# Kernel optimization log

Measured on AMD Instinct MI355X. Metric: run time of the kernel, lower is better.

The kernel has to match this reference:

```python
import jax, jax.numpy as jnp
import numpy as np

EPS = 1e-5
HEADS, K, U, M = 4, 16, 1, 11


def _bn(z, gamma, beta, mean, var):
    # z: [b, c, n]; BN in eval mode (running stats)
    inv = jax.lax.rsqrt(var + EPS)
    return (z - mean[None, :, None]) * (gamma * inv)[None, :, None] + beta[None, :, None]


def setup_inputs() -> dict:
    key = jax.random.key(0)
    ks = jax.random.split(key, 16)
    b, C, w, h = 8, 256, 64, 64
    vv = 256 // HEADS  # out_channels // heads = 64
    inp = {}
    inp['x'] = jax.random.normal(ks[0], (b, C, w, h), dtype=jnp.float32)
    sc = 1.0 / np.sqrt(C)
    inp['Wq'] = jax.random.normal(ks[1], (K * HEADS, C), dtype=jnp.float32) * sc
    inp['q_gamma'] = jnp.ones((K * HEADS,), jnp.float32)
    inp['q_beta'] = jnp.zeros((K * HEADS,), jnp.float32)
    inp['q_mean'] = jax.random.normal(ks[2], (K * HEADS,), dtype=jnp.float32) * 0.1
    inp['q_var'] = jax.random.uniform(ks[3], (K * HEADS,), minval=0.5, maxval=1.5, dtype=jnp.float32)
    inp['Wk'] = jax.random.normal(ks[4], (K * U, C), dtype=jnp.float32) * sc
    inp['Wv'] = jax.random.normal(ks[5], (vv * U, C), dtype=jnp.float32) * sc
    inp['v_gamma'] = jnp.ones((vv * U,), jnp.float32)
    inp['v_beta'] = jnp.zeros((vv * U,), jnp.float32)
    inp['v_mean'] = jax.random.normal(ks[6], (vv * U,), dtype=jnp.float32) * 0.1
    inp['v_var'] = jax.random.uniform(ks[7], (vv * U,), minval=0.5, maxval=1.5, dtype=jnp.float32)
    inp['embedding'] = jax.random.normal(ks[8], (K, U, 1, M, M), dtype=jnp.float32)
    return inp


def reference(x, Wq, q_gamma, q_beta, q_mean, q_var, Wk, Wv,
              v_gamma, v_beta, v_mean, v_var, embedding):
    b, C, w, h = x.shape
    n = w * h
    vv = Wv.shape[0] // U
    xf = x.reshape(b, C, n)

    # queries: 1x1 conv + BN -> [b, heads, k, n]
    q = _bn(jnp.einsum('oc,bcn->bon', Wq, xf), q_gamma, q_beta, q_mean, q_var)
    q = q.reshape(b, HEADS, K, n)

    # keys: 1x1 conv, softmax over spatial positions -> [b, k, u, n]
    keys = jnp.einsum('oc,bcn->bon', Wk, xf).reshape(b, K, U, n)
    sm = jax.nn.softmax(keys, axis=-1)

    # values: 1x1 conv + BN -> [b, vv, u, n]
    values = _bn(jnp.einsum('oc,bcn->bon', Wv, xf), v_gamma, v_beta, v_mean, v_var)
    values = values.reshape(b, vv, U, n)

    # content lambda
    lam_c = jnp.einsum('bkun,bvun->bkv', sm, values)          # [b, k, vv]
    y_c = jnp.einsum('bhkn,bkv->bhvn', q, lam_c)              # [b, h, vv, n]

    # position lambda via conv3d over (vv, w, h) with kernel (1, m, m)
    v5 = values.reshape(b, U, vv, w, h)                       # torch .view reinterpret
    pad = (M - 1) // 2
    lam_p = jax.lax.conv_general_dilated(
        v5, embedding, window_strides=(1, 1, 1),
        padding=((0, 0), (pad, pad), (pad, pad)),
        dimension_numbers=('NCDHW', 'OIDHW', 'NCDHW'))        # [b, k, vv, w, h]
    lam_p = lam_p.reshape(b, K, vv, n)
    y_p = jnp.einsum('bhkn,bkvn->bhvn', q, lam_p)             # [b, h, vv, n]

    out = (y_c + y_p).reshape(b, HEADS * vv, w, h)
    return out
```

## Files before the change

kernel.cpp:

```cpp
#include <hip/hip_runtime.h>
#include <math.h>

#define EPSBN 1e-5f

constexpr int B_ = 8, C_ = 256, N_ = 4096, IMG_ = 64;
constexpr int HEADS_ = 4, K_ = 16, VV_ = 64, M_ = 11, OC_ = 144;

typedef _Float16 half4 __attribute__((ext_vector_type(4)));
typedef _Float16 half8 __attribute__((ext_vector_type(8)));
typedef __fp16 fp16x2 __attribute__((ext_vector_type(2)));
typedef float f32x4 __attribute__((ext_vector_type(4)));

constexpr size_t O_WT   = 0;
constexpr size_t O_BIAS = 18432;
constexpr size_t O_EMBT = 18688;
constexpr size_t O_Q    = 24832;
constexpr size_t O_KEYS = O_Q    + 1048576;
constexpr size_t O_SM   = O_KEYS + 524288;
constexpr size_t O_VP   = O_SM   + 524288;
constexpr size_t O_VT16 = O_VP   + 1802240;
constexpr size_t O_LCP  = O_VT16 + 1048576;
constexpr size_t O_LC   = O_LCP  + 131072;

constexpr int VPROW = 88, VPPLANE = 80 * 88;

__global__ void k_prep(const float* __restrict__ Wq,
                       const float* __restrict__ qg, const float* __restrict__ qb,
                       const float* __restrict__ qm, const float* __restrict__ qv,
                       const float* __restrict__ Wk, const float* __restrict__ Wv,
                       const float* __restrict__ vg, const float* __restrict__ vb,
                       const float* __restrict__ vm, const float* __restrict__ vva,
                       const float* __restrict__ emb, float* __restrict__ ws) {
    int t = threadIdx.x, blk = blockIdx.x;
    _Float16* wf = (_Float16*)(ws + O_WT);
    int base = blk * 2304;
#pragma unroll
    for (int i = 0; i < 9; i++) {
        int idx = base + i * 256 + t;
        int o = idx >> 8, c = idx & 255;
        float w;
        if (o < 64) {
            float s = qg[o] * rsqrtf(qv[o] + EPSBN);
            w = Wq[o * 256 + c] * s;
        } else if (o < 80) {
            w = Wk[(o - 64) * 256 + c];
        } else {
            int ov = o - 80;
            float s = vg[ov] * rsqrtf(vva[ov] + EPSBN);
            w = Wv[ov * 256 + c] * s;
        }
        wf[idx] = (_Float16)w;
    }
    if (blk == 0 && t < 144) {
        float bias;
        if (t < 64) {
            float s = qg[t] * rsqrtf(qv[t] + EPSBN);
            bias = qb[t] - qm[t] * s;
        } else if (t < 80) {
            bias = 0.f;
        } else {
            int ov = t - 80;
            float s = vg[ov] * rsqrtf(vva[ov] + EPSBN);
            bias = vb[ov] - vm[ov] * s;
        }
        ws[O_BIAS + t] = bias;
    }
    if (blk == 15) {
        _Float16* ef = (_Float16*)(ws + O_EMBT);
        for (int idx = t; idx < 64 * 48; idx += 256) {
            int l = idx / 48, rem = idx % 48;
            int dp = rem >> 3, j = rem & 7;
            int k = l & 15, g = l >> 4;
            int dy = 2 * dp + (j >> 2);
            int dx = 4 * g + (j & 3);
            float v = (dy < 11 && dx < 11) ? emb[k * 121 + dy * 11 + dx] : 0.f;
            ef[idx] = (_Float16)v;
        }
    }
}

__global__ void k_zero(float* __restrict__ ws) {
    size_t i = (size_t)blockIdx.x * 256 + threadIdx.x;
    f32x4 z = {0.f, 0.f, 0.f, 0.f};
    *(f32x4*)(ws + O_VP + i * 4) = z;
}

__global__ __launch_bounds__(256) void k_proj(const float* __restrict__ x,
                                              const float* __restrict__ wsc,
                                              float* __restrict__ ws) {
    __shared__ uint WL[144 * 68];
    __shared__ uint XL[64 * 68];
    int b    = blockIdx.y;
    int pos0 = blockIdx.x * 64;
    int t    = threadIdx.x;
    int w = t >> 6, l = t & 63;
    int g = l >> 4, r = l & 15;

    f32x4 acc[9];
#pragma unroll
    for (int mf = 0; mf < 9; mf++) acc[mf] = (f32x4){0.f, 0.f, 0.f, 0.f};

    const uint* wsrc = (const uint*)(wsc + O_WT);
    const float* xb = x + (size_t)b * C_ * N_ + pos0;
    union u2h { uint2 u; half4 h; };

    for (int kh = 0; kh < 2; kh++) {
        if (kh) __syncthreads();
#pragma unroll
        for (int i = 0; i < 9; i++) {
            int idx = t + i * 256;
            int o = idx >> 4, c4 = idx & 15;
            uint4 wv = *(const uint4*)(wsrc + o * 128 + kh * 64 + c4 * 4);
            *(uint4*)&WL[o * 68 + c4 * 4] = wv;
        }
#pragma unroll
        for (int i = 0; i < 4; i++) {
            int idx = t + i * 256;
            int cl = idx >> 4, p4 = idx & 15;
            float4 a0 = *(const float4*)(xb + (size_t)(2 * (64 * kh + cl)) * N_ + 4 * p4);
            float4 a1 = *(const float4*)(xb + (size_t)(2 * (64 * kh + cl) + 1) * N_ + 4 * p4);
            union { _Float16 h[2]; uint u; } pk;
#pragma unroll
            for (int j = 0; j < 4; j++) {
                float v0 = (j == 0) ? a0.x : (j == 1) ? a0.y : (j == 2) ? a0.z : a0.w;
                float v1 = (j == 0) ? a1.x : (j == 1) ? a1.y : (j == 2) ? a1.z : a1.w;
                pk.h[0] = (_Float16)v0; pk.h[1] = (_Float16)v1;
                XL[(4 * p4 + j) * 68 + cl] = pk.u;
            }
        }
        __syncthreads();

        for (int ks = 0; ks < 8; ks++) {
            int cu = 8 * ks + 2 * g;
            u2h bf;
            bf.u = *(const uint2*)&XL[(w * 16 + r) * 68 + cu];
#pragma unroll
            for (int mf = 0; mf < 9; mf++) {
                u2h af;
                af.u = *(const uint2*)&WL[(16 * mf + r) * 68 + cu];
                acc[mf] = __builtin_amdgcn_mfma_f32_16x16x16f16(af.h, bf.h, acc[mf], 0, 0, 0);
            }
        }
    }

    int pos = pos0 + w * 16 + r;
#pragma unroll
    for (int mf = 0; mf < 9; mf++) {
        float4 bias4 = *(const float4*)(wsc + O_BIAS + 16 * mf + 4 * g);
        f32x4 a = acc[mf];
        float rv0 = a[0] + bias4.x, rv1 = a[1] + bias4.y;
        float rv2 = a[2] + bias4.z, rv3 = a[3] + bias4.w;
        if (mf < 4) {
            union { fp16x2 h[2]; uint2 u; } pk;
            pk.h[0] = __builtin_amdgcn_cvt_pkrtz(rv0, rv1);
            pk.h[1] = __builtin_amdgcn_cvt_pkrtz(rv2, rv3);
            ((uint2*)(ws + O_Q))[((size_t)(b * 16 + 4 * mf + g)) * N_ + pos] = pk.u;
        } else if (mf == 4) {
            int ch0 = 16 * mf + 4 * g;
            float* kp = ws + O_KEYS + ((size_t)(b * 16 + (ch0 - 64))) * N_ + pos;
            kp[0] = rv0; kp[(size_t)N_] = rv1; kp[2 * (size_t)N_] = rv2; kp[3 * (size_t)N_] = rv3;
        } else {
            int ov = 16 * mf + 4 * g - 80;
            int y = pos >> 6, xx = pos & 63;
            _Float16* vp = (_Float16*)(ws + O_VP) +
                           ((size_t)(b * 64 + ov)) * VPPLANE + (size_t)(y + 8) * VPROW + (xx + 8);
            vp[0] = (_Float16)rv0; vp[VPPLANE] = (_Float16)rv1;
            vp[2 * VPPLANE] = (_Float16)rv2; vp[3 * VPPLANE] = (_Float16)rv3;
            union { fp16x2 h[2]; uint2 u; } pk;
            pk.h[0] = __builtin_amdgcn_cvt_pkrtz(rv0, rv1);
            pk.h[1] = __builtin_amdgcn_cvt_pkrtz(rv2, rv3);
            ((uint2*)(ws + O_VT16))[((size_t)b * N_ + pos) * 16 + 4 * (mf - 5) + g] = pk.u;
        }
    }
}

__global__ __launch_bounds__(1024) void k_softmax(float* __restrict__ ws) {
    int row = blockIdx.x;
    const float* src = ws + O_KEYS + (size_t)row * N_;
    float*       dst = ws + O_SM   + (size_t)row * N_;
    int t = threadIdx.x;

    float4 r = *(const float4*)(src + t * 4);

    float m = fmaxf(fmaxf(r.x, r.y), fmaxf(r.z, r.w));
    for (int off = 32; off > 0; off >>= 1) m = fmaxf(m, __shfl_xor(m, off));
    __shared__ float redm[16];
    __shared__ float reds[16];
    if ((t & 63) == 0) redm[t >> 6] = m;
    __syncthreads();
    m = redm[0];
#pragma unroll
    for (int i = 1; i < 16; i++) m = fmaxf(m, redm[i]);

    r.x = expf(r.x - m); r.y = expf(r.y - m);
    r.z = expf(r.z - m); r.w = expf(r.w - m);
    float s = r.x + r.y + r.z + r.w;
    for (int off = 32; off > 0; off >>= 1) s += __shfl_xor(s, off);
    if ((t & 63) == 0) reds[t >> 6] = s;
    __syncthreads();
    s = reds[0];
#pragma unroll
    for (int i = 1; i < 16; i++) s += reds[i];
    float inv = 1.f / s;
    r.x *= inv; r.y *= inv; r.z *= inv; r.w *= inv;
    *(float4*)(dst + t * 4) = r;
}

__global__ __launch_bounds__(256) void k_lamc(float* __restrict__ ws) {
    int b  = blockIdx.x >> 4;
    int ch = blockIdx.x & 15;
    int n0 = ch * 256;
    __shared__ float sms[16 * 256];
    int t = threadIdx.x;
    for (int i = 0; i < 16; i++) {
        int idx = t + i * 256;
        int k = idx >> 8, n = idx & 255;
        sms[idx] = ws[O_SM + ((size_t)(b * 16 + k)) * N_ + n0 + n];
    }
    __syncthreads();

    int v  = t & 63;
    int kg = __builtin_amdgcn_readfirstlane(t >> 6);
    float acc[4] = {0.f, 0.f, 0.f, 0.f};
    const _Float16* vt = (const _Float16*)(ws + O_VT16) + ((size_t)b * N_ + n0) * 64 + v;
    for (int n = 0; n < 256; n++) {
        float val = (float)vt[(size_t)n * 64];
#pragma unroll
        for (int j = 0; j < 4; j++) acc[j] += sms[(kg * 4 + j) * 256 + n] * val;
    }
#pragma unroll
    for (int j = 0; j < 4; j++)
        ws[O_LCP + ((size_t)(b * 16 + ch) * 16 + kg * 4 + j) * 64 + v] = acc[j];
}

__global__ void k_lcred(float* __restrict__ ws) {
    int b = blockIdx.x, t = threadIdx.x;
    float s = 0.f;
    for (int c = 0; c < 16; c++)
        s += ws[O_LCP + ((size_t)(b * 16 + c)) * 1024 + t];
    ws[O_LC + (size_t)b * 1024 + t] = s;
}

__global__ __launch_bounds__(256, 4) void k_out(const float* __restrict__ wsc,
                                                float* __restrict__ out) {
    __shared__ ushort vt[2][4][19][84];
    int ytile = blockIdx.x;
    int vc    = blockIdx.y;
    int b     = blockIdx.z;
    int y0 = ytile * 8, v0 = vc * 4;
    int t = threadIdx.x;
    int w = t >> 6, l = t & 63;
    int g = l >> 4, nb = l & 15;

    float4 lc4[4];
#pragma unroll
    for (int i = 0; i < 4; i++)
        lc4[i] = *(const float4*)(wsc + O_LC + ((size_t)(b * 16 + 4 * g + i)) * 64 + v0);

    union AF { uint4 u; half8 h; } af[6];
    {
        const uint4* ap = (const uint4*)((const _Float16*)(wsc + O_EMBT) + (size_t)l * 48);
#pragma unroll
        for (int dp = 0; dp < 6; dp++) af[dp].u = ap[dp];
    }

    const ushort* vpb = (const ushort*)(wsc + O_VP) + (size_t)(b * 64 + v0) * VPPLANE;
    for (int T = t; T < 1596; T += 256) {
        int v = T / 399, rem = T % 399;
        int r = rem / 21, qd = rem % 21;
        const ushort* src = vpb + (size_t)v * VPPLANE + (size_t)(y0 + 3 + r) * VPROW + 4 * qd;
        uint2 u01 = *(const uint2*)src;
        uint2 u23 = *(const uint2*)(src + 4);
        *(uint2*)&vt[0][v][r][4 * qd] = u01;
        uint lo = (u01.x >> 16) | (u01.y << 16);
        uint hi = (u01.y >> 16) | (u23.x << 16);
        *(uint2*)&vt[1][v][r][4 * qd] = make_uint2(lo, hi);
    }
    __syncthreads();

    const uint* vtu = (const uint*)&vt[0][0][0][0];
    const uint2* qfp = (const uint2*)(wsc + O_Q);

#pragma unroll
    for (int xt = 0; xt < 4; xt++) {
        int X = xt * 16 + nb;
        union QH { uint2 u; fp16x2 h[2]; } qh[2][4];
#pragma unroll
        for (int yy2 = 0; yy2 < 2; yy2++) {
            int pos = (y0 + 2 * w + yy2) * 64 + X;
#pragma unroll
            for (int j = 0; j < 4; j++)
                qh[yy2][j].u = qfp[((size_t)(b * 16 + 4 * (g ^ j) + g)) * N_ + pos];
        }
        int wcol = X + 4 * g + 3;
        int cp   = wcol & 1;
        int j0u  = (wcol - cp) >> 1;

#pragma unroll
        for (int v = 0; v < 4; v++) {
            int bwin = ((cp * 4 + v) * 19 + 2 * w) * 42 + j0u;
            uint2 win[13];
#pragma unroll
            for (int i = 0; i < 13; i++) {
                win[i].x = vtu[bwin + 42 * i];
                win[i].y = vtu[bwin + 42 * i + 1];
            }

#pragma unroll
            for (int yy2 = 0; yy2 < 2; yy2++) {
                f32x4 acc = {0.f, 0.f, 0.f, 0.f};
#pragma unroll
                for (int dp = 0; dp < 6; dp++) {
                    union { uint u[4]; half8 h; } bb;
                    bb.u[0] = win[yy2 + 2 * dp].x;
                    bb.u[1] = win[yy2 + 2 * dp].y;
                    bb.u[2] = win[yy2 + 2 * dp + 1].x;
                    bb.u[3] = win[yy2 + 2 * dp + 1].y;
                    acc = __builtin_amdgcn_mfma_f32_16x16x32_f16(af[dp].h, bb.h, acc, 0, 0, 0);
                }
                float d0 = acc[0] + lc4[0][v];
                float d1 = acc[1] + lc4[1][v];
                float d2 = acc[2] + lc4[2][v];
                float d3 = acc[3] + lc4[3][v];
                fp16x2 dlo = __builtin_amdgcn_cvt_pkrtz(d0, d1);
                fp16x2 dhi = __builtin_amdgcn_cvt_pkrtz(d2, d3);
                float ph[4];
#pragma unroll
                for (int j = 0; j < 4; j++)
                    ph[j] = __builtin_amdgcn_fdot2(qh[yy2][j].h[0], dlo,
                            __builtin_amdgcn_fdot2(qh[yy2][j].h[1], dhi, 0.f, false), false);
                float sa = ph[0] + __shfl_xor(ph[1], 16);
                float sb = ph[2] + __shfl_xor(ph[3], 16);
                float o  = sa + __shfl_xor(sb, 32);
                int pos = (y0 + 2 * w + yy2) * 64 + X;
                out[((size_t)(b * 256 + g * 64 + v0 + v)) * N_ + pos] = o;
            }
        }
    }
}

extern "C" void kernel_launch(void* const* d_in, const int* in_sizes, int n_in,
                              void* d_out, int out_size, void* d_ws, size_t ws_size,
                              hipStream_t stream) {
    const float* x   = (const float*)d_in[0];
    const float* Wq  = (const float*)d_in[1];
    const float* qg  = (const float*)d_in[2];
    const float* qb  = (const float*)d_in[3];
    const float* qm  = (const float*)d_in[4];
    const float* qv  = (const float*)d_in[5];
    const float* Wk  = (const float*)d_in[6];
    const float* Wv  = (const float*)d_in[7];
    const float* vg  = (const float*)d_in[8];
    const float* vb  = (const float*)d_in[9];
    const float* vm  = (const float*)d_in[10];
    const float* vva = (const float*)d_in[11];
    const float* emb = (const float*)d_in[12];
    float* ws  = (float*)d_ws;
    float* out = (float*)d_out;

    k_prep<<<16, 256, 0, stream>>>(Wq, qg, qb, qm, qv, Wk, Wv, vg, vb, vm, vva, emb, ws);
    k_zero<<<1760, 256, 0, stream>>>(ws);
    k_proj<<<dim3(64, 8), 256, 0, stream>>>(x, ws, ws);
    k_softmax<<<128, 1024, 0, stream>>>(ws);
    k_lamc<<<128, 256, 0, stream>>>(ws);
    k_lcred<<<8, 1024, 0, stream>>>(ws);
    k_out<<<dim3(8, 16, 8), 256, 0, stream>>>(ws, out);
}
```

Baseline: 71.76 us.

## Fuse softmax normalization into lambda-content and drop transposed value copy

The workspace-zeroing kernel is folded into the prep kernel as extra blocks, removing one launch. The full softmax kernel is replaced by a kernel that only computes the inverse sum of exp(keys) per row. The exponentials are then recomputed inside k_lamc, which reads values directly from the padded fp16 value planes instead of a separately written transposed fp16 copy. k_lamc now uses 32 chunks of 128 positions, with matching changes to the partial-sum reduction. This drops the softmax output buffer and the extra value write, but exp is computed without subtracting the row max, which can overflow for large key magnitudes.

```diff
diff --git a/kernel.cpp b/kernel.cpp
--- a/kernel.cpp
+++ b/kernel.cpp
@@ -16,11 +16,10 @@
 constexpr size_t O_EMBT = 18688;
 constexpr size_t O_Q    = 24832;
 constexpr size_t O_KEYS = O_Q    + 1048576;
-constexpr size_t O_SM   = O_KEYS + 524288;
-constexpr size_t O_VP   = O_SM   + 524288;
-constexpr size_t O_VT16 = O_VP   + 1802240;
-constexpr size_t O_LCP  = O_VT16 + 1048576;
-constexpr size_t O_LC   = O_LCP  + 131072;
+constexpr size_t O_SINV = O_KEYS + 524288;
+constexpr size_t O_VP   = 1597952;
+constexpr size_t O_LCP  = O_VP   + 1802240;
+constexpr size_t O_LC   = O_LCP  + 262144;
 
 constexpr int VPROW = 88, VPPLANE = 80 * 88;
 
@@ -32,6 +31,12 @@
                        const float* __restrict__ vm, const float* __restrict__ vva,
                        const float* __restrict__ emb, float* __restrict__ ws) {
     int t = threadIdx.x, blk = blockIdx.x;
+    if (blk >= 16) {
+        size_t i = (size_t)(blk - 16) * 256 + t;
+        f32x4 z = {0.f, 0.f, 0.f, 0.f};
+        *(f32x4*)(ws + O_VP + i * 4) = z;
+        return;
+    }
     _Float16* wf = (_Float16*)(ws + O_WT);
     int base = blk * 2304;
 #pragma unroll
@@ -77,12 +82,6 @@
             ef[idx] = (_Float16)v;
         }
     }
-}
-
-__global__ void k_zero(float* __restrict__ ws) {
-    size_t i = (size_t)blockIdx.x * 256 + threadIdx.x;
-    f32x4 z = {0.f, 0.f, 0.f, 0.f};
-    *(f32x4*)(ws + O_VP + i * 4) = z;
 }
 
 __global__ __launch_bounds__(256) void k_proj(const float* __restrict__ x,
@@ -166,78 +165,85 @@
                            ((size_t)(b * 64 + ov)) * VPPLANE + (size_t)(y + 8) * VPROW + (xx + 8);
             vp[0] = (_Float16)rv0; vp[VPPLANE] = (_Float16)rv1;
             vp[2 * VPPLANE] = (_Float16)rv2; vp[3 * VPPLANE] = (_Float16)rv3;
-            union { fp16x2 h[2]; uint2 u; } pk;
-            pk.h[0] = __builtin_amdgcn_cvt_pkrtz(rv0, rv1);
-            pk.h[1] = __builtin_amdgcn_cvt_pkrtz(rv2, rv3);
-            ((uint2*)(ws + O_VT16))[((size_t)b * N_ + pos) * 16 + 4 * (mf - 5) + g] = pk.u;
-        }
-    }
-}
-
-__global__ __launch_bounds__(1024) void k_softmax(float* __restrict__ ws) {
+        }
+    }
+}
+
+__global__ __launch_bounds__(256) void k_ssum(float* __restrict__ ws) {
     int row = blockIdx.x;
     const float* src = ws + O_KEYS + (size_t)row * N_;
-    float*       dst = ws + O_SM   + (size_t)row * N_;
     int t = threadIdx.x;
-
-    float4 r = *(const float4*)(src + t * 4);
-
-    float m = fmaxf(fmaxf(r.x, r.y), fmaxf(r.z, r.w));
-    for (int off = 32; off > 0; off >>= 1) m = fmaxf(m, __shfl_xor(m, off));
-    __shared__ float redm[16];
-    __shared__ float reds[16];
-    if ((t & 63) == 0) redm[t >> 6] = m;
-    __syncthreads();
-    m = redm[0];
-#pragma unroll
-    for (int i = 1; i < 16; i++) m = fmaxf(m, redm[i]);
-
-    r.x = expf(r.x - m); r.y = expf(r.y - m);
-    r.z = expf(r.z - m); r.w = expf(r.w - m);
-    float s = r.x + r.y + r.z + r.w;
+    float s = 0.f;
+#pragma unroll
+    for (int i = 0; i < 4; i++) {
+        float4 r = *(const float4*)(src + i * 1024 + t * 4);
+        s += expf(r.x) + expf(r.y) + expf(r.z) + expf(r.w);
+    }
     for (int off = 32; off > 0; off >>= 1) s += __shfl_xor(s, off);
+    __shared__ float reds[4];
     if ((t & 63) == 0) reds[t >> 6] = s;
     __syncthreads();
-    s = reds[0];
-#pragma unroll
-    for (int i = 1; i < 16; i++) s += reds[i];
-    float inv = 1.f / s;
-    r.x *= inv; r.y *= inv; r.z *= inv; r.w *= inv;
-    *(float4*)(dst + t * 4) = r;
+    if (t == 0)
+        ws[O_SINV + row] = 1.f / (reds[0] + reds[1] + reds[2] + reds[3]);
 }
 
 __global__ __launch_bounds__(256) void k_lamc(float* __restrict__ ws) {
-    int b  = blockIdx.x >> 4;
-    int ch = blockIdx.x & 15;
-    int n0 = ch * 256;
-    __shared__ float sms[16 * 256];
+    int b  = blockIdx.x >> 5;
+    int ch = blockIdx.x & 31;
+    int n0 = ch * 128;
+    int y0r = n0 >> 6;
+    __shared__ float ek[16 * 128];
     int t = threadIdx.x;
-    for (int i = 0; i < 16; i++) {
-        int idx = t + i * 256;
-        int k = idx >> 8, n = idx & 255;
-        sms[idx] = ws[O_SM + ((size_t)(b * 16 + k)) * N_ + n0 + n];
+#pragma unroll
+    for (int i = 0; i < 2; i++) {
+        int f4 = t + i * 256;
+        int k = f4 >> 5, nq = f4 & 31;
+        float4 kv = *(const float4*)(ws + O_KEYS + ((size_t)(b * 16 + k)) * N_ + n0 + 4 * nq);
+        float is = ws[O_SINV + b * 16 + k];
+        float4 e;
+        e.x = expf(kv.x) * is; e.y = expf(kv.y) * is;
+        e.z = expf(kv.z) * is; e.w = expf(kv.w) * is;
+        *(float4*)&ek[k * 128 + 4 * nq] = e;
     }
     __syncthreads();
 
     int v  = t & 63;
     int kg = __builtin_amdgcn_readfirstlane(t >> 6);
     float acc[4] = {0.f, 0.f, 0.f, 0.f};
-    const _Float16* vt = (const _Float16*)(ws + O_VT16) + ((size_t)b * N_ + n0) * 64 + v;
-    for (int n = 0; n < 256; n++) {
-        float val = (float)vt[(size_t)n * 64];
-#pragma unroll
-        for (int j = 0; j < 4; j++) acc[j] += sms[(kg * 4 + j) * 256 + n] * val;
+    const _Float16* vp = (const _Float16*)(ws + O_VP) +
+                         (size_t)(b * 64 + v) * VPPLANE + (size_t)(y0r + 8) * VPROW + 8;
+#pragma unroll
+    for (int r = 0; r < 2; r++) {
+        union U4 { uint4 q; _Float16 h[8]; } u[8];
+#pragma unroll
+        for (int iu = 0; iu < 8; iu++)
+            u[iu].q = *(const uint4*)(vp + (size_t)r * VPROW + 8 * iu);
+#pragma unroll
+        for (int xq = 0; xq < 16; xq++) {
+            float4 e0 = *(const float4*)&ek[(kg * 4 + 0) * 128 + r * 64 + 4 * xq];
+            float4 e1 = *(const float4*)&ek[(kg * 4 + 1) * 128 + r * 64 + 4 * xq];
+            float4 e2 = *(const float4*)&ek[(kg * 4 + 2) * 128 + r * 64 + 4 * xq];
+            float4 e3 = *(const float4*)&ek[(kg * 4 + 3) * 128 + r * 64 + 4 * xq];
+            float v0 = (float)u[xq >> 1].h[(xq & 1) * 4 + 0];
+            float v1 = (float)u[xq >> 1].h[(xq & 1) * 4 + 1];
+            float v2 = (float)u[xq >> 1].h[(xq & 1) * 4 + 2];
+            float v3 = (float)u[xq >> 1].h[(xq & 1) * 4 + 3];
+            acc[0] += e0.x * v0 + e0.y * v1 + e0.z * v2 + e0.w * v3;
+            acc[1] += e1.x * v0 + e1.y * v1 + e1.z * v2 + e1.w * v3;
+            acc[2] += e2.x * v0 + e2.y * v1 + e2.z * v2 + e2.w * v3;
+            acc[3] += e3.x * v0 + e3.y * v1 + e3.z * v2 + e3.w * v3;
+        }
     }
 #pragma unroll
     for (int j = 0; j < 4; j++)
-        ws[O_LCP + ((size_t)(b * 16 + ch) * 16 + kg * 4 + j) * 64 + v] = acc[j];
+        ws[O_LCP + ((size_t)(b * 32 + ch) * 16 + kg * 4 + j) * 64 + v] = acc[j];
 }
 
 __global__ void k_lcred(float* __restrict__ ws) {
     int b = blockIdx.x, t = threadIdx.x;
     float s = 0.f;
-    for (int c = 0; c < 16; c++)
-        s += ws[O_LCP + ((size_t)(b * 16 + c)) * 1024 + t];
+    for (int c = 0; c < 32; c++)
+        s += ws[O_LCP + ((size_t)(b * 32 + c)) * 1024 + t];
     ws[O_LC + (size_t)b * 1024 + t] = s;
 }
 
@@ -358,11 +364,10 @@
     float* ws  = (float*)d_ws;
     float* out = (float*)d_out;
 
-    k_prep<<<16, 256, 0, stream>>>(Wq, qg, qb, qm, qv, Wk, Wv, vg, vb, vm, vva, emb, ws);
-    k_zero<<<1760, 256, 0, stream>>>(ws);
+    k_prep<<<1776, 256, 0, stream>>>(Wq, qg, qb, qm, qv, Wk, Wv, vg, vb, vm, vva, emb, ws);
     k_proj<<<dim3(64, 8), 256, 0, stream>>>(x, ws, ws);
-    k_softmax<<<128, 1024, 0, stream>>>(ws);
-    k_lamc<<<128, 256, 0, stream>>>(ws);
+    k_ssum<<<128, 256, 0, stream>>>(ws);
+    k_lamc<<<256, 256, 0, stream>>>(ws);
     k_lcred<<<8, 1024, 0, stream>>>(ws);
     k_out<<<dim3(8, 16, 8), 256, 0, stream>>>(ws, out);
 }
```

New measurement: 61.59 us. 1.17x faster.
